# Kernel tuning notes

Hardware: AMD Instinct MI355X
Metric: run time of the kernel (lower is better)

Reference implementation:

```python
import jax, jax.numpy as jnp
import numpy as np

B, S, D = 2, 2048, 1024
H = 16
HD = D // H  # head_dim = 64


def _xavier(key, shape):
    fan_out, fan_in = shape
    bound = jnp.sqrt(6.0 / (fan_in + fan_out))
    return jax.random.uniform(key, shape, jnp.float32, -bound, bound)


def setup_inputs() -> dict:
    key = jax.random.key(0)
    kx, kqkv, ko = jax.random.split(key, 3)
    x = jax.random.normal(kx, (B, S, D), jnp.float32)
    # torch nn.Linear stores weight as [out, in]; we keep that layout and use x @ W.T
    W_qkv = _xavier(kqkv, (3 * D, D))
    b_qkv = jnp.zeros((3 * D,), jnp.float32)
    W_o = _xavier(ko, (D, D))
    b_o = jnp.zeros((D,), jnp.float32)
    return {"x": x, "W_qkv": W_qkv, "b_qkv": b_qkv, "W_o": W_o, "b_o": b_o}


def reference(x, W_qkv, b_qkv, W_o, b_o):
    b, s, d = x.shape
    h, hd = H, HD
    # qkv projection: [b, s, 3d]
    qkv = jnp.einsum("bsd,ed->bse", x, W_qkv) + b_qkv
    # [b, s, h, 3*hd] -> [b, h, s, 3*hd]
    qkv = qkv.reshape(b, s, h, 3 * hd).transpose(0, 2, 1, 3)
    q, k, v = jnp.split(qkv, 3, axis=-1)
    scale = 1.0 / jnp.sqrt(jnp.asarray(hd, x.dtype))
    logits = jnp.einsum("bhqd,bhkd->bhqk", q, k) * scale
    attn = jax.nn.softmax(logits, axis=-1)
    values = jnp.einsum("bhqk,bhkd->bhqd", attn, v)
    values = values.transpose(0, 2, 1, 3).reshape(b, s, d)
    return jnp.einsum("bsd,ed->bse", values, W_o) + b_o
```

## Files before the change

kernel.cpp:

```cpp
#include <hip/hip_runtime.h>

typedef unsigned short u16;
typedef __attribute__((ext_vector_type(8))) short bf16x8;
typedef __attribute__((ext_vector_type(4))) float f32x4;
typedef __attribute__((ext_vector_type(16))) float f32x16;
typedef __attribute__((ext_vector_type(4))) unsigned short u16x4;

__device__ __forceinline__ u16 f2bf(float f) {
    unsigned u = __float_as_uint(f);
    u = u + 0x7FFFu + ((u >> 16) & 1u);
    return (u16)(u >> 16);
}

__device__ __forceinline__ void gload16(const void* g, void* l) {
    __builtin_amdgcn_global_load_lds(
        (const __attribute__((address_space(1))) unsigned int*)g,
        (__attribute__((address_space(3))) unsigned int*)l,
        16, 0, 0);
}

__device__ __forceinline__ f32x4 mfma16(bf16x8 a, bf16x8 b, f32x4 c) {
    return __builtin_amdgcn_mfma_f32_16x16x32_bf16(a, b, c, 0, 0, 0);
}
__device__ __forceinline__ f32x16 mfma32(bf16x8 a, bf16x8 b, f32x16 c) {
    return __builtin_amdgcn_mfma_f32_32x32x16_bf16(a, b, c, 0, 0, 0);
}

__global__ __launch_bounds__(256) void cvt_all(const float* __restrict__ x,
                                               const float* __restrict__ wqkv,
                                               const float* __restrict__ wo,
                                               u16* __restrict__ dst) {
    int i = blockIdx.x * 256 + threadIdx.x;
    float4 v;
    if (i < 1048576)       v = ((const float4*)x)[i];
    else if (i < 1835008)  v = ((const float4*)wqkv)[i - 1048576];
    else                   v = ((const float4*)wo)[i - 1835008];
    u16x4 o = { f2bf(v.x), f2bf(v.y), f2bf(v.z), f2bf(v.w) };
    ((u16x4*)dst)[i] = o;
}

template <int BM, int BN, bool OUT_BF16>
__global__ __launch_bounds__(256) void gemm_bt(const u16* __restrict__ A,
                                               const u16* __restrict__ Bm,
                                               const float* __restrict__ bias,
                                               void* __restrict__ Cp,
                                               int M, int N, int K) {
    constexpr int FM = BM / 32, FN = BN / 32;
    __shared__ u16 As[BM * 64];
    __shared__ u16 Bs[BN * 64];
    const int tid = threadIdx.x, lane = tid & 63, wave = tid >> 6;
    const int wr = wave >> 1, wc = wave & 1;
    const int l15 = lane & 15, l4 = lane >> 4;

    const int nx = gridDim.x, nwg = nx * gridDim.y;
    const int id = blockIdx.y * nx + blockIdx.x;
    const int wg = (id & 7) * (nwg >> 3) + (id >> 3);
    const int m0 = (wg / nx) * BM, n0 = (wg % nx) * BN;

    f32x4 zero = {0.f, 0.f, 0.f, 0.f};
    f32x4 acc[FM][FN];
#pragma unroll
    for (int m = 0; m < FM; ++m)
#pragma unroll
        for (int n = 0; n < FN; ++n) acc[m][n] = zero;

    const int nt = K >> 6;
    for (int t = 0; t < nt; ++t) {
#pragma unroll
        for (int i = 0; i < BM / 32; ++i) {
            int c = i * 256 + tid;
            int r = c >> 3, kc = (c & 7) ^ (r & 7);
            gload16(A + (size_t)(m0 + r) * K + t * 64 + kc * 8,
                    As + (i * 256 + wave * 64) * 8);
        }
#pragma unroll
        for (int i = 0; i < BN / 32; ++i) {
            int c = i * 256 + tid;
            int r = c >> 3, kc = (c & 7) ^ (r & 7);
            gload16(Bm + (size_t)(n0 + r) * K + t * 64 + kc * 8,
                    Bs + (i * 256 + wave * 64) * 8);
        }
        __syncthreads();
#pragma unroll
        for (int kk = 0; kk < 2; ++kk) {
            bf16x8 af[FM], bfr[FN];
#pragma unroll
            for (int m = 0; m < FM; ++m) {
                int row = wr * (BM / 2) + m * 16 + l15;
                int ch = (kk * 4 + l4) ^ (row & 7);
                af[m] = *(const bf16x8*)((const char*)As + row * 128 + ch * 16);
            }
#pragma unroll
            for (int n = 0; n < FN; ++n) {
                int row = wc * (BN / 2) + n * 16 + l15;
                int ch = (kk * 4 + l4) ^ (row & 7);
                bfr[n] = *(const bf16x8*)((const char*)Bs + row * 128 + ch * 16);
            }
#pragma unroll
            for (int m = 0; m < FM; ++m)
#pragma unroll
                for (int n = 0; n < FN; ++n)
                    acc[m][n] = mfma16(af[m], bfr[n], acc[m][n]);
        }
        __syncthreads();
    }
    float bv[FN];
#pragma unroll
    for (int n = 0; n < FN; ++n) bv[n] = bias[n0 + wc * (BN / 2) + n * 16 + l15];
#pragma unroll
    for (int m = 0; m < FM; ++m) {
#pragma unroll
        for (int j = 0; j < 4; ++j) {
            size_t row = (size_t)(m0 + wr * (BM / 2) + m * 16 + l4 * 4 + j);
#pragma unroll
            for (int n = 0; n < FN; ++n) {
                int col = n0 + wc * (BN / 2) + n * 16 + l15;
                float v = acc[m][n][j] + bv[n];
                if (OUT_BF16)
                    ((u16*)Cp)[row * (size_t)N + col] = f2bf(v);
                else
                    ((float*)Cp)[row * (size_t)N + col] = v;
            }
        }
    }
}

__global__ __launch_bounds__(512) void gemm256(const u16* __restrict__ A,
                                               const u16* __restrict__ Bm,
                                               const float* __restrict__ bias,
                                               u16* __restrict__ Cp,
                                               u16* __restrict__ Vt,
                                               int M, int N, int K) {
    __shared__ __align__(16) char lds[131072];
    const int tid = threadIdx.x, lane = tid & 63, wave = tid >> 6;
    const int wr = wave >> 2, wc = wave & 3;
    const int l15 = lane & 15, l4 = lane >> 4;

    const int nx = gridDim.x, nwg = nx * gridDim.y;
    const int id = blockIdx.y * nx + blockIdx.x;
    const int wg = (id & 7) * (nwg >> 3) + (id >> 3);
    const int m0 = (wg / nx) * 256, n0 = (wg % nx) * 256;

    const u16* asrc[2][2];
    const u16* bsrc[2][2];
#pragma unroll
    for (int q = 0; q < 2; ++q)
#pragma unroll
        for (int r = 0; r < 2; ++r) {
            int c = r * 512 + tid;
            int lr = c >> 3;
            int kc = (c & 7) ^ (lr & 7);
            asrc[q][r] = A  + (size_t)(m0 + lr + (lr & 64) + q * 64) * K + kc * 8;
            bsrc[q][r] = Bm + (size_t)(n0 + lr + (lr & 96) + q * 32) * K + kc * 8;
        }
    const int sd0 = wave * 1024;
    const int sd1 = 8192 + wave * 1024;

    const int roA = (wr * 64 + l15) * 128;
    const int roB = (wc * 32 + l15) * 128;
    int ch16[2];
#pragma unroll
    for (int kk = 0; kk < 2; ++kk) ch16[kk] = ((kk * 4 + l4) ^ (l15 & 7)) * 16;

    f32x4 zero = {0.f, 0.f, 0.f, 0.f};
    f32x4 acc[2][2][4][2];
#pragma unroll
    for (int a = 0; a < 2; ++a)
#pragma unroll
        for (int b = 0; b < 2; ++b)
#pragma unroll
            for (int c = 0; c < 4; ++c)
#pragma unroll
                for (int d = 0; d < 2; ++d) acc[a][b][c][d] = zero;

#define STG_A(q, tt) { char* rb = lds + (((tt) & 1) * 32768) + (q) * 16384;          \
        gload16(asrc[q][0] + (size_t)(tt) * 64, rb + sd0);                            \
        gload16(asrc[q][1] + (size_t)(tt) * 64, rb + sd1); }
#define STG_B(q, tt) { char* rb = lds + 65536 + (((tt) & 1) * 32768) + (q) * 16384;  \
        gload16(bsrc[q][0] + (size_t)(tt) * 64, rb + sd0);                            \
        gload16(bsrc[q][1] + (size_t)(tt) * 64, rb + sd1); }
#define MFMA_PH(MH, NH) {                                                             \
        __builtin_amdgcn_s_setprio(1);                                                \
        _Pragma("unroll")                                                             \
        for (int fm = 0; fm < 4; ++fm)                                                \
            _Pragma("unroll")                                                         \
            for (int fn = 0; fn < 2; ++fn)                                            \
                _Pragma("unroll")                                                     \
                for (int kk = 0; kk < 2; ++kk)                                        \
                    acc[MH][NH][fm][fn] =                                             \
                        mfma16(af[fm][kk], bfr[NH][fn][kk], acc[MH][NH][fm][fn]);     \
        __builtin_amdgcn_s_setprio(0); }

    STG_A(0, 0); STG_B(0, 0); STG_A(1, 0); STG_B(1, 0);
    asm volatile("s_waitcnt vmcnt(4)" ::: "memory");
    asm volatile("s_barrier" ::: "memory");

    bf16x8 af[4][2], bfr[2][2][2];
    const int nt = K >> 6;
    for (int t = 0; t < nt; ++t) {
        const char* Ab = lds + (t & 1) * 32768;
        const char* Bb = lds + 65536 + (t & 1) * 32768;
#pragma unroll
        for (int fm = 0; fm < 4; ++fm)
#pragma unroll
            for (int kk = 0; kk < 2; ++kk)
                af[fm][kk] = *(const bf16x8*)(Ab + roA + fm * 2048 + ch16[kk]);
#pragma unroll
        for (int fn = 0; fn < 2; ++fn)
#pragma unroll
            for (int kk = 0; kk < 2; ++kk)
                bfr[0][fn][kk] = *(const bf16x8*)(Bb + roB + fn * 2048 + ch16[kk]);
        if (t < nt - 1) STG_A(0, t + 1);
        asm volatile("s_barrier" ::: "memory");
        MFMA_PH(0, 0);
        asm volatile("s_barrier" ::: "memory");
#pragma unroll
        for (int fn = 0; fn < 2; ++fn)
#pragma unroll
            for (int kk = 0; kk < 2; ++kk)
                bfr[1][fn][kk] = *(const bf16x8*)(Bb + 16384 + roB + fn * 2048 + ch16[kk]);
        if (t < nt - 1) STG_B(0, t + 1);
        asm volatile("s_barrier" ::: "memory");
        MFMA_PH(0, 1);
        if (t < nt - 1) asm volatile("s_waitcnt vmcnt(4)" ::: "memory");
        else            asm volatile("s_waitcnt vmcnt(0)" ::: "memory");
        asm volatile("s_barrier" ::: "memory");
#pragma unroll
        for (int fm = 0; fm < 4; ++fm)
#pragma unroll
            for (int kk = 0; kk < 2; ++kk)
                af[fm][kk] = *(const bf16x8*)(Ab + 16384 + roA + fm * 2048 + ch16[kk]);
        if (t < nt - 1) STG_A(1, t + 1);
        asm volatile("s_barrier" ::: "memory");
        MFMA_PH(1, 0);
        asm volatile("s_barrier" ::: "memory");
        if (t < nt - 1) STG_B(1, t + 1);
        asm volatile("s_barrier" ::: "memory");
        MFMA_PH(1, 1);
        if (t < nt - 1) asm volatile("s_waitcnt vmcnt(4)" ::: "memory");
        asm volatile("s_barrier" ::: "memory");
    }
#undef STG_A
#undef STG_B
#undef MFMA_PH

    float bv[2][2];
#pragma unroll
    for (int nh = 0; nh < 2; ++nh)
#pragma unroll
        for (int fn = 0; fn < 2; ++fn)
            bv[nh][fn] = bias[n0 + wc * 64 + nh * 32 + fn * 16 + l15];
#pragma unroll
    for (int mh = 0; mh < 2; ++mh)
#pragma unroll
        for (int fm = 0; fm < 4; ++fm)
#pragma unroll
            for (int j = 0; j < 4; ++j) {
                size_t row = (size_t)(m0 + wr * 128 + mh * 64 + fm * 16 + l4 * 4 + j);
#pragma unroll
                for (int nh = 0; nh < 2; ++nh)
#pragma unroll
                    for (int fn = 0; fn < 2; ++fn) {
                        int col = n0 + wc * 64 + nh * 32 + fn * 16 + l15;
                        Cp[row * (size_t)N + col] =
                            f2bf(acc[mh][nh][fm][fn][j] + bv[nh][fn]);
                    }
            }

    const int b_ = m0 >> 11, s0_ = m0 & 2047;
    const int hmin = (n0 + 63) / 192;
    const int nV = ((hmin + 1) * 192 + 128 < n0 + 256) ? 128 : 64;
#pragma unroll
    for (int nh = 0; nh < 2; ++nh)
#pragma unroll
        for (int fn = 0; fn < 2; ++fn) {
            int col = n0 + wc * 64 + nh * 32 + fn * 16 + l15;
            int hh = col / 192;
            int dd = col - hh * 192 - 128;
            if (dd >= 0) {
                int vl = (hh - hmin) * 64 + dd;
#pragma unroll
                for (int mh = 0; mh < 2; ++mh)
#pragma unroll
                    for (int fm = 0; fm < 4; ++fm) {
                        int r0 = wr * 128 + mh * 64 + fm * 16 + l4 * 4;
                        u16x4 w = { f2bf(acc[mh][nh][fm][fn][0] + bv[nh][fn]),
                                    f2bf(acc[mh][nh][fm][fn][1] + bv[nh][fn]),
                                    f2bf(acc[mh][nh][fm][fn][2] + bv[nh][fn]),
                                    f2bf(acc[mh][nh][fm][fn][3] + bv[nh][fn]) };
                        *(u16x4*)(lds + vl * 520 + r0 * 2) = w;
                    }
            }
        }
    __syncthreads();
    {
        size_t vt_base = ((size_t)(b_ * 16 + hmin) * 64) * 2048 + s0_;
        int nchunks = nV * 64;
        for (int c = tid; c < nchunks; c += 512) {
            int vl = c >> 6, sl = c & 63;
            u16x4 w = *(const u16x4*)(lds + vl * 520 + sl * 8);
            *(u16x4*)(Vt + (size_t)vl * 2048 + vt_base + sl * 4) = w;
        }
    }
}

__global__ __launch_bounds__(512, 4) void attn_kernel(const u16* __restrict__ qkv,
                                                      const u16* __restrict__ Vt,
                                                      u16* __restrict__ vals) {
    __shared__ __align__(16) char lds[65536];
    const int L = blockIdx.x;
    const int ord = L >> 3;
    const int hb = (L & 7) * 4 + (ord >> 4);
    const int qt = ord & 15;
    const int h = hb & 15, b = hb >> 4;
    const int tid = threadIdx.x, lane = tid & 63, wave = tid >> 6;
    const int gtid = tid & 255, qsub = wave & 3, kvh = wave >> 2;
    const int l31 = lane & 31, hi = lane >> 5;
    const float S2E = 0.18033688f;

    const u16* qbase = qkv + (size_t)(b * 2048 + qt * 128 + qsub * 32 + l31) * 3072 + h * 192;
    bf16x8 Qf[4];
#pragma unroll
    for (int ks = 0; ks < 4; ++ks) {
        bf16x8 q = *(const bf16x8*)(qbase + ks * 16 + hi * 8);
#pragma unroll
        for (int j = 0; j < 8; ++j) {
            float f = __uint_as_float(((unsigned)(u16)q[j]) << 16) * S2E;
            q[j] = (short)f2bf(f);
        }
        Qf[ks] = q;
    }

    bf16x8 ones;
#pragma unroll
    for (int j = 0; j < 8; ++j) ones[j] = (short)0x3F80;

    const u16* kp[2];
    const u16* vp[2];
    int dst[2];
#pragma unroll
    for (int i = 0; i < 2; ++i) {
        int c = i * 256 + gtid;
        int fi = c >> 6, dl = c & 63;
        int mm = fi >> 2, ks = fi & 3;
        int row = mm * 32 + (dl & 31);
        int col = ks * 16 + (dl >> 5) * 8;
        kp[i] = qkv + (size_t)(b * 2048 + kvh * 1024 + row) * 3072 + h * 192 + 64 + col;
        vp[i] = Vt + ((size_t)((b * 16 + h) * 64 + row)) * 2048 + kvh * 1024 + col;
        dst[i] = fi * 512;
    }
    u16* Kst = (u16*)lds + kvh * 8192;
    u16* Vst = (u16*)lds + 16384 + kvh * 8192;

    f32x16 accO[2], accL;
#pragma unroll
    for (int md = 0; md < 2; ++md)
#pragma unroll
        for (int r = 0; r < 16; ++r) accO[md][r] = 0.f;
#pragma unroll
    for (int r = 0; r < 16; ++r) accL[r] = 0.f;

    const char* KsL = (const char*)Kst + lane * 16;
    const char* VsL = (const char*)Vst + lane * 16;

#pragma unroll
    for (int i = 0; i < 2; ++i) gload16(kp[i], Kst + dst[i]);
#pragma unroll
    for (int i = 0; i < 2; ++i) gload16(vp[i], Vst + dst[i]);
#pragma unroll
    for (int i = 0; i < 2; ++i) { kp[i] += 64 * 3072; vp[i] += 64; }

    for (int t = 0; t < 16; ++t) {
        asm volatile("s_waitcnt vmcnt(0)" ::: "memory");
        asm volatile("s_barrier" ::: "memory");

        if (t < 15) {
            u16* kd = Kst + ((t + 1) & 1) * 4096;
            u16* vd = Vst + ((t + 1) & 1) * 4096;
#pragma unroll
            for (int i = 0; i < 2; ++i) gload16(kp[i], kd + dst[i]);
#pragma unroll
            for (int i = 0; i < 2; ++i) gload16(vp[i], vd + dst[i]);
#pragma unroll
            for (int i = 0; i < 2; ++i) { kp[i] += 64 * 3072; vp[i] += 64; }
        }

        const char* Kb = KsL + (t & 1) * 8192;
        const char* Vb = VsL + (t & 1) * 8192;

        f32x16 sc[2];
        __builtin_amdgcn_s_setprio(1);
#pragma unroll
        for (int m = 0; m < 2; ++m) {
            f32x16 c;
#pragma unroll
            for (int r = 0; r < 16; ++r) c[r] = 0.f;
#pragma unroll
            for (int ks = 0; ks < 4; ++ks) {
                bf16x8 kf = *(const bf16x8*)(Kb + (m * 4 + ks) * 1024);
                c = mfma32(kf, Qf[ks], c);
            }
            sc[m] = c;
        }
        __builtin_amdgcn_s_setprio(0);

        bf16x8 Pf[4];
#pragma unroll
        for (int r = 0; r < 16; ++r)
            sc[0][r] = __builtin_amdgcn_exp2f(sc[0][r]);
        {
            unsigned W0[4], W1[4];
#pragma unroll
            for (int g = 0; g < 4; ++g) {
                asm("v_cvt_pk_bf16_f32 %0, %1, %2"
                    : "=v"(W0[g]) : "v"(sc[0][4 * g + 0]), "v"(sc[0][4 * g + 1]));
                asm("v_cvt_pk_bf16_f32 %0, %1, %2"
                    : "=v"(W1[g]) : "v"(sc[0][4 * g + 2]), "v"(sc[0][4 * g + 3]));
            }
#pragma unroll
            for (int kpair = 0; kpair < 2; ++kpair) {
                unsigned xa = W0[2 * kpair], ya = W0[2 * kpair + 1];
                unsigned xb = W1[2 * kpair], yb = W1[2 * kpair + 1];
                asm volatile("v_permlane32_swap_b32 %0, %1" : "+v"(xa), "+v"(ya));
                asm volatile("v_permlane32_swap_b32 %0, %1" : "+v"(xb), "+v"(yb));
                union { unsigned w[4]; bf16x8 v; } u;
                u.w[0] = xa; u.w[1] = xb; u.w[2] = ya; u.w[3] = yb;
                Pf[kpair] = u.v;
            }
        }

#pragma unroll
        for (int md = 0; md < 2; ++md) {
            f32x16 c = accO[md];
#pragma unroll
            for (int ks = 0; ks < 2; ++ks) {
                bf16x8 vf = *(const bf16x8*)(Vb + (md * 4 + ks) * 1024);
                c = mfma32(vf, Pf[ks], c);
            }
            accO[md] = c;
        }
#pragma unroll
        for (int ks = 0; ks < 2; ++ks)
            accL = mfma32(ones, Pf[ks], accL);

#pragma unroll
        for (int r = 0; r < 16; ++r)
            sc[1][r] = __builtin_amdgcn_exp2f(sc[1][r]);
        {
            unsigned W0[4], W1[4];
#pragma unroll
            for (int g = 0; g < 4; ++g) {
                asm("v_cvt_pk_bf16_f32 %0, %1, %2"
                    : "=v"(W0[g]) : "v"(sc[1][4 * g + 0]), "v"(sc[1][4 * g + 1]));
                asm("v_cvt_pk_bf16_f32 %0, %1, %2"
                    : "=v"(W1[g]) : "v"(sc[1][4 * g + 2]), "v"(sc[1][4 * g + 3]));
            }
#pragma unroll
            for (int kpair = 0; kpair < 2; ++kpair) {
                unsigned xa = W0[2 * kpair], ya = W0[2 * kpair + 1];
                unsigned xb = W1[2 * kpair], yb = W1[2 * kpair + 1];
                asm volatile("v_permlane32_swap_b32 %0, %1" : "+v"(xa), "+v"(ya));
                asm volatile("v_permlane32_swap_b32 %0, %1" : "+v"(xb), "+v"(yb));
                union { unsigned w[4]; bf16x8 v; } u;
                u.w[0] = xa; u.w[1] = xb; u.w[2] = ya; u.w[3] = yb;
                Pf[2 + kpair] = u.v;
            }
        }

#pragma unroll
        for (int md = 0; md < 2; ++md) {
            f32x16 c = accO[md];
#pragma unroll
            for (int ks = 2; ks < 4; ++ks) {
                bf16x8 vf = *(const bf16x8*)(Vb + (md * 4 + ks) * 1024);
                c = mfma32(vf, Pf[ks], c);
            }
            accO[md] = c;
        }
#pragma unroll
        for (int ks = 2; ks < 4; ++ks)
            accL = mfma32(ones, Pf[ks], accL);
    }

    float lt = accL[0];

    float* MO = (float*)lds;
    float* ML = (float*)(lds + 32768);
    __syncthreads();
    if (kvh == 1) {
#pragma unroll
        for (int md = 0; md < 2; ++md)
#pragma unroll
            for (int g = 0; g < 4; ++g) {
                f32x4 w = { accO[md][4 * g + 0], accO[md][4 * g + 1],
                            accO[md][4 * g + 2], accO[md][4 * g + 3] };
                *(f32x4*)&MO[(qsub * 64 + lane) * 32 + md * 16 + 4 * g] = w;
            }
        ML[qsub * 64 + lane] = lt;
    }
    __syncthreads();
    if (kvh == 0) {
        float inv = 1.f / (lt + ML[qsub * 64 + lane]);
        size_t rowoff = (size_t)(b * 2048 + qt * 128 + qsub * 32 + l31) * 1024 + h * 64;
#pragma unroll
        for (int md = 0; md < 2; ++md)
#pragma unroll
            for (int g = 0; g < 4; ++g) {
                f32x4 w = *(const f32x4*)&MO[(qsub * 64 + lane) * 32 + md * 16 + 4 * g];
                u16x4 o = { f2bf((accO[md][4 * g + 0] + w[0]) * inv),
                            f2bf((accO[md][4 * g + 1] + w[1]) * inv),
                            f2bf((accO[md][4 * g + 2] + w[2]) * inv),
                            f2bf((accO[md][4 * g + 3] + w[3]) * inv) };
                *(u16x4*)(vals + rowoff + md * 32 + 8 * g + 4 * hi) = o;
            }
    }
}

extern "C" void kernel_launch(void* const* d_in, const int* in_sizes, int n_in,
                              void* d_out, int out_size, void* d_ws, size_t ws_size,
                              hipStream_t stream) {
    const float* x    = (const float*)d_in[0];
    const float* Wqkv = (const float*)d_in[1];
    const float* bqkv = (const float*)d_in[2];
    const float* Wo   = (const float*)d_in[3];
    const float* bo   = (const float*)d_in[4];
    float* out = (float*)d_out;

    char* ws = (char*)d_ws;
    u16* x_bf    = (u16*)(ws);
    u16* Wqkv_bf = (u16*)(ws + 8388608);
    u16* Wo_bf   = (u16*)(ws + 14680064);
    u16* qkv_bf  = (u16*)(ws + 16777216);
    u16* Vt      = (u16*)(ws + 41943040);
    u16* vals    = (u16*)(ws + 50331648);

    cvt_all<<<8192, 256, 0, stream>>>(x, Wqkv, Wo, x_bf);

    gemm256<<<dim3(12, 16), 512, 0, stream>>>(x_bf, Wqkv_bf, bqkv, qkv_bf, Vt,
                                              4096, 3072, 1024);

    attn_kernel<<<512, 512, 0, stream>>>(qkv_bf, Vt, vals);

    gemm_bt<128, 64, false><<<dim3(16, 32), 256, 0, stream>>>(vals, Wo_bf, bo,
                                                              (void*)out, 4096, 1024, 1024);
}
```

Before: 114.5 us.

## Double-buffer GEMM LDS tiles and raise wave priority around attention MFMAs

The bf16 GEMM kernel now keeps two LDS buffers for A and B. The next K-tile is issued with global_load_lds while the current tile is being multiplied, and the loop uses one waitcnt plus one barrier per iteration instead of two __syncthreads. Separately, the attention kernel brackets its PV and row-sum MFMA blocks with s_setprio(1)/s_setprio(0) so those waves get issue priority. Double buffering doubles the GEMM's shared memory, which may lower occupancy. Relying on a single barrier to protect buffer reuse is correct only if every wave reaches it before the buffer being read is overwritten.

```diff
diff --git a/kernel.cpp b/kernel.cpp
--- a/kernel.cpp
+++ b/kernel.cpp
@@ -46,8 +46,8 @@
                                                void* __restrict__ Cp,
                                                int M, int N, int K) {
     constexpr int FM = BM / 32, FN = BN / 32;
-    __shared__ u16 As[BM * 64];
-    __shared__ u16 Bs[BN * 64];
+    __shared__ u16 As[2][BM * 64];
+    __shared__ u16 Bs[2][BN * 64];
     const int tid = threadIdx.x, lane = tid & 63, wave = tid >> 6;
     const int wr = wave >> 1, wc = wave & 1;
     const int l15 = lane & 15, l4 = lane >> 4;
@@ -64,23 +64,30 @@
 #pragma unroll
         for (int n = 0; n < FN; ++n) acc[m][n] = zero;
 
+#define STAGE_BT(tt, buf) {                                                 \
+    _Pragma("unroll")                                                       \
+    for (int i = 0; i < BM / 32; ++i) {                                     \
+        int c = i * 256 + tid;                                              \
+        int r = c >> 3, kc = (c & 7) ^ (r & 7);                             \
+        gload16(A + (size_t)(m0 + r) * K + (tt) * 64 + kc * 8,              \
+                &As[buf][(i * 256 + wave * 64) * 8]);                       \
+    }                                                                       \
+    _Pragma("unroll")                                                       \
+    for (int i = 0; i < BN / 32; ++i) {                                     \
+        int c = i * 256 + tid;                                              \
+        int r = c >> 3, kc = (c & 7) ^ (r & 7);                             \
+        gload16(Bm + (size_t)(n0 + r) * K + (tt) * 64 + kc * 8,             \
+                &Bs[buf][(i * 256 + wave * 64) * 8]);                       \
+    } }
+
     const int nt = K >> 6;
+    STAGE_BT(0, 0);
     for (int t = 0; t < nt; ++t) {
-#pragma unroll
-        for (int i = 0; i < BM / 32; ++i) {
-            int c = i * 256 + tid;
-            int r = c >> 3, kc = (c & 7) ^ (r & 7);
-            gload16(A + (size_t)(m0 + r) * K + t * 64 + kc * 8,
-                    As + (i * 256 + wave * 64) * 8);
-        }
-#pragma unroll
-        for (int i = 0; i < BN / 32; ++i) {
-            int c = i * 256 + tid;
-            int r = c >> 3, kc = (c & 7) ^ (r & 7);
-            gload16(Bm + (size_t)(n0 + r) * K + t * 64 + kc * 8,
-                    Bs + (i * 256 + wave * 64) * 8);
-        }
-        __syncthreads();
+        asm volatile("s_waitcnt vmcnt(0)" ::: "memory");
+        asm volatile("s_barrier" ::: "memory");
+        if (t < nt - 1) { STAGE_BT(t + 1, (t + 1) & 1); }
+        const char* Asb = (const char*)As[t & 1];
+        const char* Bsb = (const char*)Bs[t & 1];
 #pragma unroll
         for (int kk = 0; kk < 2; ++kk) {
             bf16x8 af[FM], bfr[FN];
@@ -88,13 +95,13 @@
             for (int m = 0; m < FM; ++m) {
                 int row = wr * (BM / 2) + m * 16 + l15;
                 int ch = (kk * 4 + l4) ^ (row & 7);
-                af[m] = *(const bf16x8*)((const char*)As + row * 128 + ch * 16);
+                af[m] = *(const bf16x8*)(Asb + row * 128 + ch * 16);
             }
 #pragma unroll
             for (int n = 0; n < FN; ++n) {
                 int row = wc * (BN / 2) + n * 16 + l15;
                 int ch = (kk * 4 + l4) ^ (row & 7);
-                bfr[n] = *(const bf16x8*)((const char*)Bs + row * 128 + ch * 16);
+                bfr[n] = *(const bf16x8*)(Bsb + row * 128 + ch * 16);
             }
 #pragma unroll
             for (int m = 0; m < FM; ++m)
@@ -102,8 +109,8 @@
                 for (int n = 0; n < FN; ++n)
                     acc[m][n] = mfma16(af[m], bfr[n], acc[m][n]);
         }
-        __syncthreads();
-    }
+    }
+#undef STAGE_BT
     float bv[FN];
 #pragma unroll
     for (int n = 0; n < FN; ++n) bv[n] = bias[n0 + wc * (BN / 2) + n * 16 + l15];
@@ -429,6 +436,7 @@
             }
         }
 
+        __builtin_amdgcn_s_setprio(1);
 #pragma unroll
         for (int md = 0; md < 2; ++md) {
             f32x16 c = accO[md];
@@ -442,6 +450,7 @@
 #pragma unroll
         for (int ks = 0; ks < 2; ++ks)
             accL = mfma32(ones, Pf[ks], accL);
+        __builtin_amdgcn_s_setprio(0);
 
 #pragma unroll
         for (int r = 0; r < 16; ++r)
@@ -467,6 +476,7 @@
             }
         }
 
+        __builtin_amdgcn_s_setprio(1);
 #pragma unroll
         for (int md = 0; md < 2; ++md) {
             f32x16 c = accO[md];
@@ -480,6 +490,7 @@
 #pragma unroll
         for (int ks = 2; ks < 4; ++ks)
             accL = mfma32(ones, Pf[ks], accL);
+        __builtin_amdgcn_s_setprio(0);
     }
 
     float lt = accL[0];
```

After: 113.4 us. Within noise of the previous version (-0.9%).
